# Optimization experiments

Measured on AMD Instinct MI355X. Metric: run time of the kernel, lower is better.

Reference implementation:

```python
import jax, jax.numpy as jnp
import numpy as np

N, E, C1, E2, C2, B = 30000, 400000, 15000, 100000, 7500, 16
FV, FE, NC = 6, 3, 10


def _lin(k, i, o):
    kw, kb = jax.random.split(k)
    s = 1.0 / np.sqrt(i)
    w = jax.random.uniform(kw, (i, o), jnp.float32, -s, s)
    b = jax.random.uniform(kb, (o,), jnp.float32, -s, s)
    return w, b


def setup_inputs() -> dict:
    key = jax.random.key(0)
    ks = jax.random.split(key, 20)
    inp = {}
    inp["x"] = jax.random.normal(ks[0], (N, FV), jnp.float32)
    inp["edge_attr"] = jax.random.uniform(ks[1], (E, FE), jnp.float32)
    inp["pos"] = jax.random.uniform(ks[2], (N, 3), jnp.float32)
    inp["edge_index"] = jax.random.randint(ks[3], (2, E), 0, N)
    inp["batch"] = jnp.sort(jax.random.randint(ks[4], (N,), 0, B))
    inp["cluster1"] = jax.random.randint(ks[5], (N,), 0, C1)
    inp["edge_index2"] = jax.random.randint(ks[6], (2, E2), 0, C1)
    inp["cluster2"] = jax.random.randint(ks[7], (C1,), 0, C2)
    inp["w1a"], inp["b1a"] = _lin(ks[8], FE, 25)
    inp["w1b"], inp["b1b"] = _lin(ks[9], 25, 32 * FV)
    inp["root1"] = jax.random.normal(ks[10], (FV, 32), jnp.float32) / np.sqrt(FV)
    inp["bias1"] = jnp.zeros((32,), jnp.float32)
    inp["w2a"], inp["b2a"] = _lin(ks[11], 3, 25)
    inp["w2b"], inp["b2b"] = _lin(ks[12], 25, 32 * 64)
    inp["root2"] = jax.random.normal(ks[13], (32, 64), jnp.float32) / np.sqrt(32)
    inp["bias2"] = jnp.zeros((64,), jnp.float32)
    inp["fc1_w"], inp["fc1_b"] = _lin(ks[14], 64, 128)
    inp["fc2_w"], inp["fc2_b"] = _lin(ks[15], 128, NC)
    return inp


def _seg_mean(v, idx, n):
    s = jax.ops.segment_sum(v, idx, num_segments=n)
    c = jax.ops.segment_sum(jnp.ones(idx.shape, v.dtype), idx, num_segments=n)
    return s / jnp.maximum(c, 1.0)[:, None]


def _seg_max(v, idx, n):
    m = jax.ops.segment_max(v, idx, num_segments=n)
    return jnp.where(jnp.isfinite(m), m, 0.0)  # empty clusters -> 0


def _nnconv(x, src, dst, ea, wa, ba, wb, bb, root, bias, n, ci, co):
    # per-edge weight matrix from edge MLP: [E, ci, co]
    W = (jax.nn.relu(ea @ wa + ba) @ wb + bb).reshape(-1, ci, co)
    msg = jnp.einsum('ei,eio->eo', x[src], W)  # gather + per-edge matmul
    return _seg_mean(msg, dst, n) + x @ root + bias  # scatter-mean + root


def _cartesian(pos, src, dst):
    cart = pos[src] - pos[dst]
    return cart / (2.0 * jnp.max(jnp.abs(cart))) + 0.5  # T.Cartesian(norm=True)


def reference(x, edge_attr, pos, w1a, b1a, w1b, b1b, root1, bias1,
              w2a, b2a, w2b, b2b, root2, bias2, fc1_w, fc1_b, fc2_w, fc2_b,
              edge_index, batch, cluster1, edge_index2, cluster2):
    src1, dst1 = edge_index[0], edge_index[1]
    x1 = jax.nn.elu(_nnconv(x, src1, dst1, edge_attr, w1a, b1a, w1b, b1b,
                            root1, bias1, N, FV, 32))
    # max_pool with precomputed graclus cluster assignment
    xp = _seg_max(x1, cluster1, C1)
    posp = _seg_mean(pos, cluster1, C1)
    batchp = jnp.maximum(jax.ops.segment_max(batch, cluster1, num_segments=C1), 0)
    src2, dst2 = edge_index2[0], edge_index2[1]
    ea2 = _cartesian(posp, src2, dst2)
    x2 = jax.nn.elu(_nnconv(xp, src2, dst2, ea2, w2a, b2a, w2b, b2b,
                            root2, bias2, C1, 32, 64))
    # max_pool_x with second cluster assignment
    x3 = _seg_max(x2, cluster2, C2)
    batch2 = jnp.maximum(jax.ops.segment_max(batchp, cluster2, num_segments=C2), 0)
    g = _seg_mean(x3, batch2, B)  # global mean pool -> [B, 64]
    h = jax.nn.elu(g @ fc1_w + fc1_b)
    # dropout is identity in eval mode
    return jax.nn.log_softmax(h @ fc2_w + fc2_b, axis=1)
```

## Files before the change

kernel.cpp:

```cpp
#include <hip/hip_runtime.h>
#include <hip/hip_bf16.h>

#define Nn 30000
#define Ee 400000
#define C1n 15000
#define E2n 100000
#define C2n 7500
#define Bb 16

#define OFF_SUM1   0
#define OFF_CNT1   960000
#define OFF_XPKEY  990000
#define OFF_POSSUM 1470000
#define OFF_CNTC1  1515000
#define OFF_BPMAX  1530000
#define OFF_SUM2   1545000
#define OFF_CNT2   2505000
#define OFF_X3KEY  2520000
#define OFF_B2MAX  3000000
#define OFF_GSUM   3007500
#define OFF_GCNT   3008524
#define OFF_MAXABS 3008540
#define ZERO_ELEMS 3008544
#define OFF_X1     3008544
#define OFF_XP     3968544
#define OFF_POSP   4448544
#define OFF_CART   4493544
#define OFF_H2     4793544
#define OFF_T2     7293544
#define OFF_X2     19773544

typedef __attribute__((ext_vector_type(8))) short short8;
typedef __attribute__((ext_vector_type(4))) float f32x4;

__device__ __forceinline__ unsigned fkey(float f) {
    unsigned u = __float_as_uint(f);
    return (u >> 31) ? ~u : (u | 0x80000000u);
}
__device__ __forceinline__ float funkey(unsigned k) {
    unsigned u = (k >> 31) ? (k ^ 0x80000000u) : ~k;
    return __uint_as_float(u);
}
__device__ __forceinline__ float elu(float a) { return a > 0.f ? a : expm1f(a); }

__device__ __forceinline__ unsigned short f2bf(float f) {
    unsigned u = __float_as_uint(f);
    unsigned lsb = (u >> 16) & 1u;
    u += 0x7fffu + lsb;
    return (unsigned short)(u >> 16);
}
__device__ __forceinline__ float bf2f(unsigned short s) {
    return __uint_as_float(((unsigned)s) << 16);
}

__global__ __launch_bounds__(256, 4) void conv1_mfma(
    const float* __restrict__ x, const float* __restrict__ ea,
    const int* __restrict__ ei,
    const float* __restrict__ w1a, const float* __restrict__ b1a,
    const float* __restrict__ w1b, const float* __restrict__ b1b,
    float* __restrict__ sum1, float* __restrict__ cnt1) {
    const int lane = threadIdx.x & 63;
    const int m = lane & 15;
    const int q = lane >> 4;

    short8 Bf[6][2];
#pragma unroll
    for (int s = 0; s < 6; ++s) {
#pragma unroll
        for (int h = 0; h < 2; ++h) {
            short8 pk;
#pragma unroll
            for (int j = 0; j < 8; ++j) {
                const int u = s * 8 + j;
                const int t = u / 6, i = u % 6;
                float w = 0.f;
                if (t < 7) {
                    int k = q + 4 * t;
                    int col = h * 16 + m;
                    if (k < 25)       w = w1b[k * 192 + i * 32 + col];
                    else if (k == 25) w = b1b[i * 32 + col];
                }
                pk[j] = (short)f2bf(w);
            }
            Bf[s][h] = pk;
        }
    }

    const int wid = (blockIdx.x * blockDim.x + threadIdx.x) >> 6;
    const int nw = (gridDim.x * blockDim.x) >> 6;
    for (int tile = wid; tile < Ee / 16; tile += nw) {
        const int e0 = tile * 16;
        const int e = e0 + m;
        const int src = ei[e];
        const float ea0 = ea[e * 3], ea1 = ea[e * 3 + 1], ea2 = ea[e * 3 + 2];
        float xs[6];
#pragma unroll
        for (int i = 0; i < 6; ++i) xs[i] = x[src * 6 + i];

        float hh[8];
#pragma unroll
        for (int t = 0; t < 6; ++t) {
            int k = q + 4 * t;
            float a = b1a[k] + ea0 * w1a[k] + ea1 * w1a[25 + k] + ea2 * w1a[50 + k];
            hh[t] = fmaxf(a, 0.f);
        }
        {
            if (q == 0) {
                float a = b1a[24] + ea0 * w1a[24] + ea1 * w1a[49] + ea2 * w1a[74];
                hh[6] = fmaxf(a, 0.f);
            } else hh[6] = (q == 1) ? 1.f : 0.f;
        }
        hh[7] = 0.f;

        f32x4 acc0 = {0.f, 0.f, 0.f, 0.f}, acc1 = {0.f, 0.f, 0.f, 0.f};
#pragma unroll
        for (int s = 0; s < 6; ++s) {
            short8 av;
#pragma unroll
            for (int j = 0; j < 8; ++j) {
                const int u = s * 8 + j;
                av[j] = (short)f2bf(hh[u / 6] * xs[u % 6]);
            }
            acc0 = __builtin_amdgcn_mfma_f32_16x16x32_bf16(av, Bf[s][0], acc0, 0, 0, 0);
            acc1 = __builtin_amdgcn_mfma_f32_16x16x32_bf16(av, Bf[s][1], acc1, 0, 0, 0);
        }

#pragma unroll
        for (int r = 0; r < 4; ++r) {
            const int row = q * 4 + r;
            const int dstr = ei[Ee + e0 + row];
            atomicAdd(&sum1[dstr * 32 + m], acc0[r]);
            atomicAdd(&sum1[dstr * 32 + 16 + m], acc1[r]);
        }
        if (q == 0) {
            const int dstm = ei[Ee + e0 + m];
            atomicAdd(&cnt1[dstm], 1.f);
        }
    }
}

__global__ void x1_kernel(const float* __restrict__ sum1, const float* __restrict__ cnt1,
                          const float* __restrict__ x, const float* __restrict__ root1,
                          const float* __restrict__ bias1, float* __restrict__ x1) {
    int t = blockIdx.x * 256 + threadIdx.x;
    if (t >= Nn * 32) return;
    int n = t >> 5, o = t & 31;
    float a = sum1[t] / fmaxf(cnt1[n], 1.f) + bias1[o];
#pragma unroll
    for (int i = 0; i < 6; ++i) a += x[n * 6 + i] * root1[i * 32 + o];
    x1[t] = elu(a);
}

__global__ void pool1_kernel(const float* __restrict__ x1, const float* __restrict__ pos,
                             const int* __restrict__ batch, const int* __restrict__ cluster1,
                             unsigned* __restrict__ xpkey, float* __restrict__ possum,
                             float* __restrict__ cntc1, int* __restrict__ bpmax) {
    int t = blockIdx.x * 256 + threadIdx.x;
    if (t >= Nn * 32) return;
    int n = t >> 5, o = t & 31;
    int c = cluster1[n];
    atomicMax(&xpkey[c * 32 + o], fkey(x1[t]));
    if (o == 0) {
#pragma unroll
        for (int j = 0; j < 3; ++j) atomicAdd(&possum[c * 3 + j], pos[n * 3 + j]);
        atomicAdd(&cntc1[c], 1.f);
        atomicMax(&bpmax[c], batch[n]);
    }
}

__global__ void pool1_final(const unsigned* __restrict__ xpkey, const float* __restrict__ possum,
                            const float* __restrict__ cntc1, float* __restrict__ xp,
                            float* __restrict__ posp) {
    int t = blockIdx.x * 256 + threadIdx.x;
    if (t >= C1n * 32) return;
    int c = t >> 5, o = t & 31;
    unsigned k = xpkey[t];
    xp[t] = k ? funkey(k) : 0.f;
    if (o < 3) posp[c * 3 + o] = possum[c * 3 + o] / fmaxf(cntc1[c], 1.f);
}

__global__ void cart_kernel(const float* __restrict__ posp, const int* __restrict__ ei2,
                            float* __restrict__ cart, unsigned* __restrict__ maxabs) {
    int e = blockIdx.x * 256 + threadIdx.x;
    float mx = 0.f;
    if (e < E2n) {
        int s = ei2[e], d = ei2[E2n + e];
#pragma unroll
        for (int j = 0; j < 3; ++j) {
            float cv = posp[s * 3 + j] - posp[d * 3 + j];
            cart[e * 3 + j] = cv;
            mx = fmaxf(mx, fabsf(cv));
        }
    }
#pragma unroll
    for (int off = 32; off > 0; off >>= 1) mx = fmaxf(mx, __shfl_xor(mx, off));
    if ((threadIdx.x & 63) == 0) atomicMax(maxabs, __float_as_uint(mx));
}

__global__ void h2_kernel(const float* __restrict__ cart, const unsigned* __restrict__ maxabs,
                          const float* __restrict__ w2a, const float* __restrict__ b2a,
                          float* __restrict__ h2) {
    int t = blockIdx.x * 256 + threadIdx.x;
    if (t >= E2n * 25) return;
    int e = t / 25, k = t % 25;
    float inv = 0.5f / __uint_as_float(maxabs[0]);
    float a = b2a[k];
#pragma unroll
    for (int j = 0; j < 3; ++j) a += (cart[e * 3 + j] * inv + 0.5f) * w2a[j * 25 + k];
    h2[t] = fmaxf(a, 0.f);
}

__global__ __launch_bounds__(256) void t2_gemm(const float* __restrict__ xp,
                                               const float* __restrict__ w2b,
                                               const float* __restrict__ b2b,
                                               unsigned short* __restrict__ T2) {
    __shared__ float As[256 * 36];
    __shared__ float Bs[32][68];
    const int bm = blockIdx.x * 256;
    const int bn = blockIdx.y * 64;
    const int t = threadIdx.x;
#pragma unroll
    for (int r = 0; r < 8; ++r) {
        int qd = t + r * 256;
        int row = qd >> 3, i4 = (qd & 7) * 4;
        int n = bm + row;
        float4 v = make_float4(0.f, 0.f, 0.f, 0.f);
        if (n < C1n) v = *reinterpret_cast<const float4*>(&xp[n * 32 + i4]);
        *reinterpret_cast<float4*>(&As[row * 36 + i4]) = v;
    }
#pragma unroll
    for (int r = 0; r < 8; ++r) {
        int idx = t + r * 256;
        int i = idx >> 6, nn = idx & 63;
        int col = bn + nn;
        float v;
        if (col < 1600) { int k = col >> 6, o = col & 63; v = w2b[k * 2048 + i * 64 + o]; }
        else            { v = b2b[i * 64 + (col & 63)]; }
        Bs[i][nn] = v;
    }
    __syncthreads();
    const int tn4 = (t & 15) * 4;
    const int tr = t >> 4;
    for (int it = 0; it < 8; ++it) {
        int r0 = it * 32 + tr, r1 = r0 + 16;
        float a0[32], a1[32];
#pragma unroll
        for (int qd = 0; qd < 8; ++qd) {
            *reinterpret_cast<float4*>(&a0[qd * 4]) = *reinterpret_cast<const float4*>(&As[r0 * 36 + qd * 4]);
            *reinterpret_cast<float4*>(&a1[qd * 4]) = *reinterpret_cast<const float4*>(&As[r1 * 36 + qd * 4]);
        }
        float acc0[4] = {0.f, 0.f, 0.f, 0.f}, acc1[4] = {0.f, 0.f, 0.f, 0.f};
#pragma unroll
        for (int k = 0; k < 32; ++k) {
            float4 bv = *reinterpret_cast<const float4*>(&Bs[k][tn4]);
            acc0[0] += a0[k] * bv.x; acc0[1] += a0[k] * bv.y;
            acc0[2] += a0[k] * bv.z; acc0[3] += a0[k] * bv.w;
            acc1[0] += a1[k] * bv.x; acc1[1] += a1[k] * bv.y;
            acc1[2] += a1[k] * bv.z; acc1[3] += a1[k] * bv.w;
        }
        int row0 = bm + r0, row1 = bm + r1;
        if (row0 < C1n) {
            union { unsigned short us[4]; uint2 v; } pk;
            pk.us[0] = f2bf(acc0[0]); pk.us[1] = f2bf(acc0[1]);
            pk.us[2] = f2bf(acc0[2]); pk.us[3] = f2bf(acc0[3]);
            *reinterpret_cast<uint2*>(&T2[(size_t)row0 * 1664 + bn + tn4]) = pk.v;
        }
        if (row1 < C1n) {
            union { unsigned short us[4]; uint2 v; } pk;
            pk.us[0] = f2bf(acc1[0]); pk.us[1] = f2bf(acc1[1]);
            pk.us[2] = f2bf(acc1[2]); pk.us[3] = f2bf(acc1[3]);
            *reinterpret_cast<uint2*>(&T2[(size_t)row1 * 1664 + bn + tn4]) = pk.v;
        }
    }
}

__global__ void conv2_msg(const unsigned short* __restrict__ T2, const float* __restrict__ h2,
                          const int* __restrict__ ei2, float* __restrict__ sum2,
                          float* __restrict__ cnt2) {
    int t = blockIdx.x * 256 + threadIdx.x;
    if (t >= E2n * 64) return;
    int e = t >> 6, o = t & 63;
    int src = ei2[e], dst = ei2[E2n + e];
    const unsigned short* Trow = T2 + (size_t)src * 1664;
    float acc = bf2f(Trow[25 * 64 + o]);
#pragma unroll
    for (int k = 0; k < 25; ++k) acc += h2[e * 25 + k] * bf2f(Trow[k * 64 + o]);
    atomicAdd(&sum2[dst * 64 + o], acc);
    if (o == 0) atomicAdd(&cnt2[dst], 1.f);
}

__global__ void x2_kernel(const float* __restrict__ sum2, const float* __restrict__ cnt2,
                          const float* __restrict__ xp, const float* __restrict__ root2,
                          const float* __restrict__ bias2, float* __restrict__ x2) {
    int t = blockIdx.x * 256 + threadIdx.x;
    if (t >= C1n * 64) return;
    int c = t >> 6, o = t & 63;
    float a = sum2[t] / fmaxf(cnt2[c], 1.f) + bias2[o];
#pragma unroll
    for (int i = 0; i < 32; ++i) a += xp[c * 32 + i] * root2[i * 64 + o];
    x2[t] = elu(a);
}

__global__ void pool2_kernel(const float* __restrict__ x2, const int* __restrict__ cluster2,
                             const int* __restrict__ bpmax, unsigned* __restrict__ x3key,
                             int* __restrict__ b2max) {
    int t = blockIdx.x * 256 + threadIdx.x;
    if (t >= C1n * 64) return;
    int c = t >> 6, o = t & 63;
    int c2 = cluster2[c];
    atomicMax(&x3key[c2 * 64 + o], fkey(x2[t]));
    if (o == 0) atomicMax(&b2max[c2], bpmax[c]);
}

__global__ __launch_bounds__(256) void gacc_kernel(
    const unsigned* __restrict__ x3key, const int* __restrict__ b2max,
    float* __restrict__ gsum, float* __restrict__ gcnt) {
    __shared__ float ls[Bb * 64];
    __shared__ float lc[Bb];
    const int t = threadIdx.x;
    for (int i = t; i < Bb * 64; i += 256) ls[i] = 0.f;
    if (t < Bb) lc[t] = 0.f;
    __syncthreads();
    const int o = t & 63;
    const int cs = t >> 6;
    for (int c = blockIdx.x * 4 + cs; c < C2n; c += gridDim.x * 4) {
        int b = b2max[c];
        unsigned k = x3key[c * 64 + o];
        float v = k ? funkey(k) : 0.f;
        atomicAdd(&ls[b * 64 + o], v);
        if (o == 0) atomicAdd(&lc[b], 1.f);
    }
    __syncthreads();
    for (int i = t; i < Bb * 64; i += 256) {
        float v = ls[i];
        if (v != 0.f) atomicAdd(&gsum[i], v);
    }
    if (t < Bb) {
        float v = lc[t];
        if (v != 0.f) atomicAdd(&gcnt[t], v);
    }
}

__global__ void head_kernel(const float* __restrict__ gsum, const float* __restrict__ gcnt,
                            const float* __restrict__ fc1w, const float* __restrict__ fc1b,
                            const float* __restrict__ fc2w, const float* __restrict__ fc2b,
                            float* __restrict__ out) {
    __shared__ float g[16 * 64];
    __shared__ float hb[16 * 128];
    __shared__ float lg[16 * 10];
    __shared__ float rowm[16];
    int t = threadIdx.x;
    for (int idx = t; idx < 16 * 64; idx += 256) {
        int b = idx >> 6;
        g[idx] = gsum[idx] / fmaxf(gcnt[b], 1.f);
    }
    __syncthreads();
    for (int idx = t; idx < 16 * 128; idx += 256) {
        int b = idx >> 7, j = idx & 127;
        float a = fc1b[j];
        for (int i = 0; i < 64; ++i) a += g[b * 64 + i] * fc1w[i * 128 + j];
        hb[idx] = elu(a);
    }
    __syncthreads();
    for (int idx = t; idx < 160; idx += 256) {
        int b = idx / 10, c = idx % 10;
        float a = fc2b[c];
        for (int i = 0; i < 128; ++i) a += hb[b * 128 + i] * fc2w[i * 10 + c];
        lg[idx] = a;
    }
    __syncthreads();
    if (t < 16) {
        float m = -1e30f;
        for (int c = 0; c < 10; ++c) m = fmaxf(m, lg[t * 10 + c]);
        float s = 0.f;
        for (int c = 0; c < 10; ++c) s += expf(lg[t * 10 + c] - m);
        rowm[t] = m + logf(s);
    }
    __syncthreads();
    for (int idx = t; idx < 160; idx += 256) out[idx] = lg[idx] - rowm[idx / 10];
}

extern "C" void kernel_launch(void* const* d_in, const int* in_sizes, int n_in,
                              void* d_out, int out_size, void* d_ws, size_t ws_size,
                              hipStream_t stream) {
    const float* x     = (const float*)d_in[0];
    const float* ea    = (const float*)d_in[1];
    const float* pos   = (const float*)d_in[2];
    const int*   ei    = (const int*)d_in[3];
    const int*   batch = (const int*)d_in[4];
    const int*   cl1   = (const int*)d_in[5];
    const int*   ei2   = (const int*)d_in[6];
    const int*   cl2   = (const int*)d_in[7];
    const float* w1a   = (const float*)d_in[8];
    const float* b1a   = (const float*)d_in[9];
    const float* w1b   = (const float*)d_in[10];
    const float* b1b   = (const float*)d_in[11];
    const float* root1 = (const float*)d_in[12];
    const float* bias1 = (const float*)d_in[13];
    const float* w2a   = (const float*)d_in[14];
    const float* b2a   = (const float*)d_in[15];
    const float* w2b   = (const float*)d_in[16];
    const float* b2b   = (const float*)d_in[17];
    const float* root2 = (const float*)d_in[18];
    const float* bias2 = (const float*)d_in[19];
    const float* fc1w  = (const float*)d_in[20];
    const float* fc1b  = (const float*)d_in[21];
    const float* fc2w  = (const float*)d_in[22];
    const float* fc2b  = (const float*)d_in[23];
    float* out = (float*)d_out;

    float* ws = (float*)d_ws;
    float*    sum1   = ws + OFF_SUM1;
    float*    cnt1   = ws + OFF_CNT1;
    unsigned* xpkey  = (unsigned*)(ws + OFF_XPKEY);
    float*    possum = ws + OFF_POSSUM;
    float*    cntc1  = ws + OFF_CNTC1;
    int*      bpmax  = (int*)(ws + OFF_BPMAX);
    float*    sum2   = ws + OFF_SUM2;
    float*    cnt2   = ws + OFF_CNT2;
    unsigned* x3key  = (unsigned*)(ws + OFF_X3KEY);
    int*      b2max  = (int*)(ws + OFF_B2MAX);
    float*    gsum   = ws + OFF_GSUM;
    float*    gcnt   = ws + OFF_GCNT;
    unsigned* maxabs = (unsigned*)(ws + OFF_MAXABS);
    float*    x1     = ws + OFF_X1;
    float*    xp     = ws + OFF_XP;
    float*    posp   = ws + OFF_POSP;
    float*    cart   = ws + OFF_CART;
    float*    h2     = ws + OFF_H2;
    unsigned short* T2 = (unsigned short*)(ws + OFF_T2);
    float*    x2     = ws + OFF_X2;

    hipMemsetAsync(ws, 0, (size_t)ZERO_ELEMS * 4, stream);

    conv1_mfma<<<1024, 256, 0, stream>>>(x, ea, ei, w1a, b1a, w1b, b1b, sum1, cnt1);
    x1_kernel<<<(Nn * 32 + 255) / 256, 256, 0, stream>>>(sum1, cnt1, x, root1, bias1, x1);
    pool1_kernel<<<(Nn * 32 + 255) / 256, 256, 0, stream>>>(x1, pos, batch, cl1, xpkey, possum, cntc1, bpmax);
    pool1_final<<<(C1n * 32 + 255) / 256, 256, 0, stream>>>(xpkey, possum, cntc1, xp, posp);
    cart_kernel<<<(E2n + 255) / 256, 256, 0, stream>>>(posp, ei2, cart, maxabs);
    h2_kernel<<<(E2n * 25 + 255) / 256, 256, 0, stream>>>(cart, maxabs, w2a, b2a, h2);
    dim3 tgrid((C1n + 255) / 256, 26);
    t2_gemm<<<tgrid, 256, 0, stream>>>(xp, w2b, b2b, T2);
    conv2_msg<<<(E2n * 64 + 255) / 256, 256, 0, stream>>>(T2, h2, ei2, sum2, cnt2);
    x2_kernel<<<(C1n * 64 + 255) / 256, 256, 0, stream>>>(sum2, cnt2, xp, root2, bias2, x2);
    pool2_kernel<<<(C1n * 64 + 255) / 256, 256, 0, stream>>>(x2, cl2, bpmax, x3key, b2max);
    gacc_kernel<<<32, 256, 0, stream>>>(x3key, b2max, gsum, gcnt);
    head_kernel<<<1, 256, 0, stream>>>(gsum, gcnt, fc1w, fc1b, fc2w, fc2b, out);
}
```

Baseline: 352.6 us.

## Transpose T2 layout to per-output contiguous k and raise conv1 occupancy

The T2 intermediate is relaid out from [k][o] to [o][k padded to 32], so each conv2_msg thread loads its 26 bf16 coefficients with a few wide vector loads instead of 26 strided scalar loads. The t2_gemm grid and B-tile fill are adapted to the padded 2048-column layout, and the workspace offset for x2 moves to make room. Separately, conv1_mfma gets a higher launch-bounds occupancy hint and twice as many blocks. The padding increases T2 size and GEMM work by about a quarter, and the occupancy hint may force register spills.

```diff
diff --git a/kernel.cpp b/kernel.cpp
--- a/kernel.cpp
+++ b/kernel.cpp
@@ -28,7 +28,7 @@
 #define OFF_CART   4493544
 #define OFF_H2     4793544
 #define OFF_T2     7293544
-#define OFF_X2     19773544
+#define OFF_X2     22653544
 
 typedef __attribute__((ext_vector_type(8))) short short8;
 typedef __attribute__((ext_vector_type(4))) float f32x4;
@@ -53,7 +53,7 @@
     return __uint_as_float(((unsigned)s) << 16);
 }
 
-__global__ __launch_bounds__(256, 4) void conv1_mfma(
+__global__ __launch_bounds__(256, 8) void conv1_mfma(
     const float* __restrict__ x, const float* __restrict__ ea,
     const int* __restrict__ ei,
     const float* __restrict__ w1a, const float* __restrict__ b1a,
@@ -233,9 +233,10 @@
         int idx = t + r * 256;
         int i = idx >> 6, nn = idx & 63;
         int col = bn + nn;
-        float v;
-        if (col < 1600) { int k = col >> 6, o = col & 63; v = w2b[k * 2048 + i * 64 + o]; }
-        else            { v = b2b[i * 64 + (col & 63)]; }
+        int o = col >> 5, k = col & 31;
+        float v = 0.f;
+        if (k < 25)       v = w2b[k * 2048 + i * 64 + o];
+        else if (k == 25) v = b2b[i * 64 + o];
         Bs[i][nn] = v;
     }
     __syncthreads();
@@ -263,28 +264,41 @@
             union { unsigned short us[4]; uint2 v; } pk;
             pk.us[0] = f2bf(acc0[0]); pk.us[1] = f2bf(acc0[1]);
             pk.us[2] = f2bf(acc0[2]); pk.us[3] = f2bf(acc0[3]);
-            *reinterpret_cast<uint2*>(&T2[(size_t)row0 * 1664 + bn + tn4]) = pk.v;
+            *reinterpret_cast<uint2*>(&T2[(size_t)row0 * 2048 + bn + tn4]) = pk.v;
         }
         if (row1 < C1n) {
             union { unsigned short us[4]; uint2 v; } pk;
             pk.us[0] = f2bf(acc1[0]); pk.us[1] = f2bf(acc1[1]);
             pk.us[2] = f2bf(acc1[2]); pk.us[3] = f2bf(acc1[3]);
-            *reinterpret_cast<uint2*>(&T2[(size_t)row1 * 1664 + bn + tn4]) = pk.v;
-        }
-    }
-}
-
-__global__ void conv2_msg(const unsigned short* __restrict__ T2, const float* __restrict__ h2,
-                          const int* __restrict__ ei2, float* __restrict__ sum2,
-                          float* __restrict__ cnt2) {
+            *reinterpret_cast<uint2*>(&T2[(size_t)row1 * 2048 + bn + tn4]) = pk.v;
+        }
+    }
+}
+
+__global__ __launch_bounds__(256) void conv2_msg(
+    const unsigned short* __restrict__ T2, const float* __restrict__ h2,
+    const int* __restrict__ ei2, float* __restrict__ sum2, float* __restrict__ cnt2) {
     int t = blockIdx.x * 256 + threadIdx.x;
     if (t >= E2n * 64) return;
     int e = t >> 6, o = t & 63;
     int src = ei2[e], dst = ei2[E2n + e];
-    const unsigned short* Trow = T2 + (size_t)src * 1664;
-    float acc = bf2f(Trow[25 * 64 + o]);
-#pragma unroll
-    for (int k = 0; k < 25; ++k) acc += h2[e * 25 + k] * bf2f(Trow[k * 64 + o]);
+    const unsigned short* Tl = T2 + (size_t)src * 2048 + o * 32;
+    uint4 a0 = *reinterpret_cast<const uint4*>(Tl);
+    uint4 a1 = *reinterpret_cast<const uint4*>(Tl + 8);
+    uint4 a2 = *reinterpret_cast<const uint4*>(Tl + 16);
+    unsigned a3 = *reinterpret_cast<const unsigned*>(Tl + 24);
+    float tv[26];
+    unsigned w[13] = {a0.x, a0.y, a0.z, a0.w, a1.x, a1.y, a1.z, a1.w,
+                      a2.x, a2.y, a2.z, a2.w, a3};
+#pragma unroll
+    for (int p = 0; p < 13; ++p) {
+        tv[2 * p]     = __uint_as_float(w[p] << 16);
+        tv[2 * p + 1] = __uint_as_float(w[p] & 0xffff0000u);
+    }
+    const float* he = h2 + e * 25;
+    float acc = tv[25];
+#pragma unroll
+    for (int k = 0; k < 25; ++k) acc += he[k] * tv[k];
     atomicAdd(&sum2[dst * 64 + o], acc);
     if (o == 0) atomicAdd(&cnt2[dst], 1.f);
 }
@@ -433,13 +447,13 @@
 
     hipMemsetAsync(ws, 0, (size_t)ZERO_ELEMS * 4, stream);
 
-    conv1_mfma<<<1024, 256, 0, stream>>>(x, ea, ei, w1a, b1a, w1b, b1b, sum1, cnt1);
+    conv1_mfma<<<2048, 256, 0, stream>>>(x, ea, ei, w1a, b1a, w1b, b1b, sum1, cnt1);
     x1_kernel<<<(Nn * 32 + 255) / 256, 256, 0, stream>>>(sum1, cnt1, x, root1, bias1, x1);
     pool1_kernel<<<(Nn * 32 + 255) / 256, 256, 0, stream>>>(x1, pos, batch, cl1, xpkey, possum, cntc1, bpmax);
     pool1_final<<<(C1n * 32 + 255) / 256, 256, 0, stream>>>(xpkey, possum, cntc1, xp, posp);
     cart_kernel<<<(E2n + 255) / 256, 256, 0, stream>>>(posp, ei2, cart, maxabs);
     h2_kernel<<<(E2n * 25 + 255) / 256, 256, 0, stream>>>(cart, maxabs, w2a, b2a, h2);
-    dim3 tgrid((C1n + 255) / 256, 26);
+    dim3 tgrid((C1n + 255) / 256, 2048 / 64);
     t2_gemm<<<tgrid, 256, 0, stream>>>(xp, w2b, b2b, T2);
     conv2_msg<<<(E2n * 64 + 255) / 256, 256, 0, stream>>>(T2, h2, ei2, sum2, cnt2);
     x2_kernel<<<(C1n * 64 + 255) / 256, 256, 0, stream>>>(sum2, cnt2, xp, root2, bias2, x2);
```

After: 437.3 us. 24.0% more time.
